# Optimization experiments

Hardware: AMD Instinct MI355X
Metric: run time of the kernel (lower is better)

## Reference

```python
import jax, jax.numpy as jnp
import numpy as np

EMBED_DIM = 1024
NUM_HEADS = 16
HEAD_DIM = EMBED_DIM // NUM_HEADS


def setup_inputs() -> dict:
    key = jax.random.key(0)
    k1, k2, k3 = jax.random.split(key, 3)
    B, S = 2, 2048
    scale_in = 1.0 / np.sqrt(EMBED_DIM)
    x = jax.random.normal(k1, (B, S, EMBED_DIM), dtype=jnp.float32)
    Wqkv = jax.random.normal(k2, (EMBED_DIM, 3 * EMBED_DIM), dtype=jnp.float32) * scale_in
    bqkv = jnp.zeros((3 * EMBED_DIM,), dtype=jnp.float32)
    Wout = jax.random.normal(k3, (EMBED_DIM, EMBED_DIM), dtype=jnp.float32) * scale_in
    bout = jnp.zeros((EMBED_DIM,), dtype=jnp.float32)
    return {"x": x, "Wqkv": Wqkv, "bqkv": bqkv, "Wout": Wout, "bout": bout}


def reference(x, Wqkv, bqkv, Wout, bout):
    # Causal multi-head self-attention (dropout in eval mode = identity).
    B, S, E = x.shape
    qkv = x @ Wqkv + bqkv                                  # [B,S,3E]
    qkv = qkv.reshape(B, S, 3, NUM_HEADS, HEAD_DIM)
    qkv = jnp.transpose(qkv, (2, 0, 3, 1, 4))              # [3,B,H,S,D]
    q, k, v = qkv[0], qkv[1], qkv[2]
    scores = jnp.einsum("bhqd,bhkd->bhqk", q, k) / np.sqrt(HEAD_DIM)
    causal = jnp.tril(jnp.ones((S, S), dtype=bool))
    scores = jnp.where(causal, scores, -jnp.inf)
    attn = jax.nn.softmax(scores, axis=-1)                 # [B,H,S,S]
    out = jnp.einsum("bhqk,bhkd->bhqd", attn, v)           # [B,H,S,D]
    out = jnp.transpose(out, (0, 2, 1, 3)).reshape(B, S, E)
    return out @ Wout + bout
```

## Files before the change

kernel.cpp:

```cpp
#include <hip/hip_runtime.h>
#include <hip/hip_bf16.h>

#define BB 2
#define SS 2048
#define EE 1024
#define HH 16
#define DD 64
#define MT (BB*SS)
#define NQ (3*EE)

typedef unsigned short u16;
typedef __bf16 bf16t;
typedef bf16t bf16x8 __attribute__((ext_vector_type(8)));
typedef short short8v __attribute__((ext_vector_type(8)));
typedef float f32x4 __attribute__((ext_vector_type(4)));

#define AS1 __attribute__((address_space(1)))
#define AS3 __attribute__((address_space(3)))

__device__ __forceinline__ u16 f2b(float f) {
  unsigned u = __builtin_bit_cast(unsigned, f);
  u += 0x7FFF + ((u >> 16) & 1);
  return (u16)(u >> 16);
}

__device__ __forceinline__ unsigned cvtpk(float lo, float hi) {
  unsigned r;
  asm("v_cvt_pk_bf16_f32 %0, %1, %2" : "=v"(r) : "v"(lo), "v"(hi));
  return r;
}

__device__ __forceinline__ void gload_lds16(const void* g, void* l) {
  __builtin_amdgcn_global_load_lds((const AS1 void*)(g), (AS3 void*)(l), 16, 0, 0);
}

__device__ __forceinline__ f32x4 mfma_bf16(short8v a, short8v b, f32x4 c) {
  return __builtin_amdgcn_mfma_f32_16x16x32_bf16(
      __builtin_bit_cast(bf16x8, a), __builtin_bit_cast(bf16x8, b), c, 0, 0, 0);
}

#define QSCALE 0.18033688f

__global__ void __launch_bounds__(256) cast_kernel(const float* __restrict__ in,
                                                   u16* __restrict__ out, int n) {
  int i = (blockIdx.x * 256 + threadIdx.x) * 4;
  if (i + 3 < n) {
    float4 v = *(const float4*)(in + i);
    ushort4 o;
    o.x = f2b(v.x); o.y = f2b(v.y); o.z = f2b(v.z); o.w = f2b(v.w);
    *(ushort4*)(out + i) = o;
  }
}

__global__ void __launch_bounds__(256) transpose_kernel(const float* __restrict__ W,
                                                        u16* __restrict__ WT,
                                                        int K, int N) {
  __shared__ float t[64][65];
  int k0 = blockIdx.y * 64, n0 = blockIdx.x * 64;
  int r = threadIdx.x >> 4;
  int c4 = (threadIdx.x & 15) * 4;
#pragma unroll
  for (int i = 0; i < 4; ++i) {
    float4 v = *(const float4*)(W + (size_t)(k0 + r + i * 16) * N + n0 + c4);
    t[r + i * 16][c4 + 0] = v.x; t[r + i * 16][c4 + 1] = v.y;
    t[r + i * 16][c4 + 2] = v.z; t[r + i * 16][c4 + 3] = v.w;
  }
  __syncthreads();
#pragma unroll
  for (int i = 0; i < 4; ++i) {
    ushort4 o;
    o.x = f2b(t[c4 + 0][r + i * 16]); o.y = f2b(t[c4 + 1][r + i * 16]);
    o.z = f2b(t[c4 + 2][r + i * 16]); o.w = f2b(t[c4 + 3][r + i * 16]);
    *(ushort4*)(WT + (size_t)(n0 + r + i * 16) * K + k0 + c4) = o;
  }
}

__global__ void __launch_bounds__(256) gemm_qkv_kernel(
    const u16* __restrict__ A, const u16* __restrict__ BT,
    const float* __restrict__ bias,
    u16* __restrict__ Qs, u16* __restrict__ Ks, u16* __restrict__ Vt) {
  __shared__ u16 As[8192];
  __shared__ u16 Bs[8192];
  const int K = EE;
  int tid = threadIdx.x;
  int w = tid >> 6, lane = tid & 63;
  int g = lane >> 4, q = lane & 15;
  int m0 = blockIdx.y * 128, n0 = blockIdx.x * 128;
  int wm = (w >> 1) * 64, wn = (w & 1) * 64;

  f32x4 acc[4][4] = {};

  int r = tid >> 2;
  int kc = (tid & 3) * 8;
  const u16* ga = A + (size_t)(m0 + r) * K + kc;
  const u16* gb = BT + (size_t)(n0 + r) * K + kc;
  u16* lA0 = As + w * 512;
  u16* lA1 = As + 2048 + w * 512;
  u16* lB0 = Bs + w * 512;
  u16* lB1 = Bs + 2048 + w * 512;

  gload_lds16(ga, lA0);
  gload_lds16(ga + 64 * K, lA1);
  gload_lds16(gb, lB0);
  gload_lds16(gb + 64 * K, lB1);
  ga += 32; gb += 32;
  __syncthreads();

  int cur = 0;
  for (int k0 = 0; k0 < K; k0 += 32) {
    if (k0 + 32 < K) {
      int nx = (cur ^ 1) * 4096;
      gload_lds16(ga, lA0 + nx);
      gload_lds16(ga + 64 * K, lA1 + nx);
      gload_lds16(gb, lB0 + nx);
      gload_lds16(gb + 64 * K, lB1 + nx);
      ga += 32; gb += 32;
    }
    const u16* Ab = As + cur * 4096;
    const u16* Bb = Bs + cur * 4096;
    short8v af[4], bfv[4];
#pragma unroll
    for (int m = 0; m < 4; ++m)
      af[m] = *(const short8v*)(Ab + (wm + m * 16 + q) * 32 + g * 8);
#pragma unroll
    for (int n = 0; n < 4; ++n)
      bfv[n] = *(const short8v*)(Bb + (wn + n * 16 + q) * 32 + g * 8);
#pragma unroll
    for (int m = 0; m < 4; ++m)
#pragma unroll
      for (int n = 0; n < 4; ++n)
        acc[m][n] = mfma_bf16(af[m], bfv[n], acc[m][n]);
    __syncthreads();
    cur ^= 1;
  }

#pragma unroll
  for (int m = 0; m < 4; ++m) {
    int row0 = m0 + wm + m * 16 + g * 4;
#pragma unroll
    for (int n = 0; n < 4; ++n) {
      int col = n0 + wn + n * 16 + q;
      float bi = bias[col];
      int t = col >> 10;
      int h = (col >> 6) & 15;
      int d = col & 63;
      int b = row0 >> 11, s0 = row0 & 2047;
      size_t bh = (size_t)b * HH + h;
      if (t == 2) {
        ushort4 vv;
        vv.x = f2b(acc[m][n][0] + bi); vv.y = f2b(acc[m][n][1] + bi);
        vv.z = f2b(acc[m][n][2] + bi); vv.w = f2b(acc[m][n][3] + bi);
        *(ushort4*)&Vt[(bh * DD + d) * SS + s0] = vv;
      } else if (t == 0) {
#pragma unroll
        for (int r2 = 0; r2 < 4; ++r2)
          Qs[(bh * SS + s0 + r2) * DD + d] = f2b((acc[m][n][r2] + bi) * QSCALE);
      } else {
#pragma unroll
        for (int r2 = 0; r2 < 4; ++r2)
          Ks[(bh * SS + s0 + r2) * DD + d] = f2b(acc[m][n][r2] + bi);
      }
    }
  }
}

__global__ void __launch_bounds__(512) attn_kernel(
    const u16* __restrict__ Qg, const u16* __restrict__ Kg,
    const u16* __restrict__ Vg, u16* __restrict__ O) {
  __shared__ char lds[49152];
  const int tid = threadIdx.x;
  const int w = tid >> 6, lane = tid & 63;
  const int g = lane >> 4, q = lane & 15;
  const int bid = blockIdx.x;
  const int bh = bid & 31;
  const int p = 15 - (bid >> 5);
  const int b = bh >> 4, h = bh & 15;
  char* Pw = lds + 32768 + w * 2048;
  const int qsw = (q & 7) << 4;

  const char* Qp = (const char*)Qg + (size_t)bh * (SS * 128);
  const char* Kp = (const char*)Kg + (size_t)bh * (SS * 128);
  const char* Vp = (const char*)Vg + (size_t)bh * (SS * 128);

  const int srow = tid >> 3;
  const int ssw = ((tid & 7) * 16) ^ ((srow & 7) << 4);
  const char* Ksrc = Kp + srow * 128 + ssw;
  const char* Vsrc = Vp + (size_t)srow * (SS * 2) + ssw;
  char* Kdst = lds + w * 1024;
  char* Vdst = lds + 16384 + w * 1024;

  const int nt = 2 * p + 2;
  const int qw = p * 128 + w * 16;

  short8v aq0 = *(const short8v*)(Qp + (size_t)(qw + q) * 128 + g * 16);
  short8v aq1 = *(const short8v*)(Qp + (size_t)(qw + q) * 128 + 64 + g * 16);

  f32x4 oacc[4] = {};
  float mrun = -1e30f, lrun = 0.f;

  gload_lds16(Ksrc, Kdst);
  gload_lds16(Vsrc, Vdst);
  __syncthreads();

  for (int s = 0; s < nt; ++s) {
    const int buf = s & 1;
    if (s + 1 < nt) {
      gload_lds16(Ksrc + (size_t)(s + 1) * 8192, Kdst + (buf ^ 1) * 8192);
      gload_lds16(Vsrc + (s + 1) * 128, Vdst + (buf ^ 1) * 8192);
    }
    const int kv0 = s << 6;
    if (kv0 <= qw + 15) {
      const char* Kc = lds + buf * 8192;
      const char* Vc = lds + 16384 + buf * 8192;
      short8v kf[4][2];
#pragma unroll
      for (int cc = 0; cc < 4; ++cc) {
        const char* kb = Kc + (cc * 16 + q) * 128;
        kf[cc][0] = *(const short8v*)(kb + ((g * 16) ^ qsw));
        kf[cc][1] = *(const short8v*)(kb + ((64 + g * 16) ^ qsw));
      }
      f32x4 st[4];
#pragma unroll
      for (int cc = 0; cc < 4; ++cc) {
        f32x4 z = {};
        z = mfma_bf16(kf[cc][0], aq0, z);
        z = mfma_bf16(kf[cc][1], aq1, z);
        st[cc] = z;
      }
      short8v vf[4][2];
#pragma unroll
      for (int v = 0; v < 4; ++v) {
        const char* vb = Vc + (v * 16 + q) * 128;
        vf[v][0] = *(const short8v*)(vb + ((g * 16) ^ qsw));
        vf[v][1] = *(const short8v*)(vb + ((64 + g * 16) ^ qsw));
      }
      if (kv0 + 63 > qw) {
        int row = qw + q;
#pragma unroll
        for (int cc = 0; cc < 4; ++cc) {
          int kvb = kv0 + cc * 16 + g * 4;
#pragma unroll
          for (int r2 = 0; r2 < 4; ++r2)
            if (kvb + r2 > row) st[cc][r2] = -1e30f;
        }
      }
      f32x4 t01, t23;
#pragma unroll
      for (int r2 = 0; r2 < 4; ++r2) {
        t01[r2] = fmaxf(st[0][r2], st[1][r2]);
        t23[r2] = fmaxf(st[2][r2], st[3][r2]);
      }
      float mx = fmaxf(fmaxf(fmaxf(t01[0], t01[1]), fmaxf(t01[2], t01[3])),
                       fmaxf(fmaxf(t23[0], t23[1]), fmaxf(t23[2], t23[3])));
      mx = fmaxf(mx, __shfl_xor(mx, 16));
      mx = fmaxf(mx, __shfl_xor(mx, 32));
      if (!__all(mx - mrun <= 8.f)) {
        float mnew = fmaxf(mrun, mx);
        float alpha = exp2f(mrun - mnew);
        mrun = mnew;
        lrun *= alpha;
#pragma unroll
        for (int vfi = 0; vfi < 4; ++vfi)
#pragma unroll
          for (int r2 = 0; r2 < 4; ++r2) oacc[vfi][r2] *= alpha;
      }
      f32x4 sum4 = {};
#pragma unroll
      for (int cc = 0; cc < 4; ++cc)
#pragma unroll
        for (int r2 = 0; r2 < 4; ++r2) {
          float pv = exp2f(st[cc][r2] - mrun);
          st[cc][r2] = pv;
          sum4[r2] += pv;
        }
      float sm = (sum4[0] + sum4[1]) + (sum4[2] + sum4[3]);
      sm += __shfl_xor(sm, 16);
      sm += __shfl_xor(sm, 32);
      lrun += sm;
      char* basep = Pw + q * 128;
#pragma unroll
      for (int cc = 0; cc < 4; ++cc) {
        unsigned p01 = cvtpk(st[cc][0], st[cc][1]);
        unsigned p23 = cvtpk(st[cc][2], st[cc][3]);
        *(unsigned*)(basep + ((32 * cc + 8 * g + 0) ^ qsw)) = p01;
        *(unsigned*)(basep + ((32 * cc + 8 * g + 4) ^ qsw)) = p23;
      }
      short8v pa0 = *(const short8v*)(basep + ((g * 16) ^ qsw));
      short8v pa1 = *(const short8v*)(basep + ((64 + g * 16) ^ qsw));
#pragma unroll
      for (int vfi = 0; vfi < 4; ++vfi) {
        oacc[vfi] = mfma_bf16(vf[vfi][0], pa0, oacc[vfi]);
        oacc[vfi] = mfma_bf16(vf[vfi][1], pa1, oacc[vfi]);
      }
    }
    __syncthreads();
  }

  {
    float inv = 1.0f / lrun;
    int row = qw + q;
    char* obase = (char*)O + (((size_t)b * SS + row) * EE + h * 64) * 2;
#pragma unroll
    for (int vfi = 0; vfi < 4; ++vfi) {
      uint2 o;
      o.x = cvtpk(oacc[vfi][0] * inv, oacc[vfi][1] * inv);
      o.y = cvtpk(oacc[vfi][2] * inv, oacc[vfi][3] * inv);
      *(uint2*)(obase + (vfi * 16 + g * 4) * 2) = o;
    }
  }
}

__global__ void __launch_bounds__(256) gemm_out_kernel(
    const u16* __restrict__ A, const u16* __restrict__ BT,
    const float* __restrict__ bias, float* __restrict__ Cout) {
  __shared__ u16 As[8192];
  __shared__ u16 Bs[8192];
  const int K = EE;
  int tid = threadIdx.x;
  int w = tid >> 6, lane = tid & 63;
  int g = lane >> 4, q = lane & 15;
  int m0 = blockIdx.y * 128, n0 = blockIdx.x * 128;
  int wm = (w >> 1) * 64, wn = (w & 1) * 64;

  f32x4 acc[4][4] = {};

  int r = tid >> 2;
  int kc = (tid & 3) * 8;
  const u16* ga = A + (size_t)(m0 + r) * K + kc;
  const u16* gb = BT + (size_t)(n0 + r) * K + kc;
  u16* lA0 = As + w * 512;
  u16* lA1 = As + 2048 + w * 512;
  u16* lB0 = Bs + w * 512;
  u16* lB1 = Bs + 2048 + w * 512;

  gload_lds16(ga, lA0);
  gload_lds16(ga + 64 * K, lA1);
  gload_lds16(gb, lB0);
  gload_lds16(gb + 64 * K, lB1);
  ga += 32; gb += 32;
  __syncthreads();

  int cur = 0;
  for (int k0 = 0; k0 < K; k0 += 32) {
    if (k0 + 32 < K) {
      int nx = (cur ^ 1) * 4096;
      gload_lds16(ga, lA0 + nx);
      gload_lds16(ga + 64 * K, lA1 + nx);
      gload_lds16(gb, lB0 + nx);
      gload_lds16(gb + 64 * K, lB1 + nx);
      ga += 32; gb += 32;
    }
    const u16* Ab = As + cur * 4096;
    const u16* Bb = Bs + cur * 4096;
    short8v af[4], bfv[4];
#pragma unroll
    for (int m = 0; m < 4; ++m)
      af[m] = *(const short8v*)(Ab + (wm + m * 16 + q) * 32 + g * 8);
#pragma unroll
    for (int n = 0; n < 4; ++n)
      bfv[n] = *(const short8v*)(Bb + (wn + n * 16 + q) * 32 + g * 8);
#pragma unroll
    for (int m = 0; m < 4; ++m)
#pragma unroll
      for (int n = 0; n < 4; ++n)
        acc[m][n] = mfma_bf16(af[m], bfv[n], acc[m][n]);
    __syncthreads();
    cur ^= 1;
  }

#pragma unroll
  for (int m = 0; m < 4; ++m) {
    int row0 = m0 + wm + m * 16 + g * 4;
#pragma unroll
    for (int n = 0; n < 4; ++n) {
      int col = n0 + wn + n * 16 + q;
      float bi = bias[col];
#pragma unroll
      for (int r2 = 0; r2 < 4; ++r2) {
        int row = row0 + r2;
        Cout[(size_t)row * EE + col] = acc[m][n][r2] + bi;
      }
    }
  }
}

extern "C" void kernel_launch(void* const* d_in, const int* in_sizes, int n_in,
                              void* d_out, int out_size, void* d_ws, size_t ws_size,
                              hipStream_t stream) {
  (void)in_sizes; (void)n_in; (void)out_size; (void)ws_size;
  const float* x    = (const float*)d_in[0];
  const float* Wqkv = (const float*)d_in[1];
  const float* bqkv = (const float*)d_in[2];
  const float* Wout = (const float*)d_in[3];
  const float* bout = (const float*)d_in[4];
  float* out = (float*)d_out;

  char* p = (char*)d_ws;
  u16* xb  = (u16*)p; p += (size_t)MT * EE * 2;
  u16* wqT = (u16*)p; p += (size_t)NQ * EE * 2;
  u16* woT = (u16*)p; p += (size_t)EE * EE * 2;
  u16* Qs  = (u16*)p; p += (size_t)BB * HH * SS * DD * 2;
  u16* Ks  = (u16*)p; p += (size_t)BB * HH * SS * DD * 2;
  u16* Vt  = (u16*)p; p += (size_t)BB * HH * DD * SS * 2;
  u16* Ob  = (u16*)p; p += (size_t)MT * EE * 2;

  cast_kernel<<<dim3((MT * EE / 4) / 256), dim3(256), 0, stream>>>(x, xb, MT * EE);
  transpose_kernel<<<dim3(NQ / 64, EE / 64), dim3(256), 0, stream>>>(Wqkv, wqT, EE, NQ);
  transpose_kernel<<<dim3(EE / 64, EE / 64), dim3(256), 0, stream>>>(Wout, woT, EE, EE);
  gemm_qkv_kernel<<<dim3(NQ / 128, MT / 128), dim3(256), 0, stream>>>(xb, wqT, bqkv, Qs, Ks, Vt);
  attn_kernel<<<dim3(512), dim3(512), 0, stream>>>(Qs, Ks, Vt, Ob);
  gemm_out_kernel<<<dim3(EE / 128, MT / 128), dim3(256), 0, stream>>>(Ob, woT, bout, out);
}
```

Measured before the change: 121.1 us.

## Split KV range across two wave halves with paired causal chunks and LDS merge

The attention kernel now uses 1024-thread blocks (256 blocks). Each block processes two 256-row query chunks (c and 7-c) so every block does the same amount of causal work. Within a block the two halves of the waves each take half of the KV tiles, and their softmax states and partial outputs are merged through LDS at the end. Each wave now handles 32 query rows, so every K/V fragment read from LDS feeds twice the MFMA work. In exchange it needs about 98KB of LDS and more registers per thread, adds merge synchronisation, and launches fewer, larger blocks, which may lower occupancy.

```diff
diff --git a/kernel.cpp b/kernel.cpp
--- a/kernel.cpp
+++ b/kernel.cpp
@@ -164,149 +164,196 @@
   }
 }
 
-__global__ void __launch_bounds__(512) attn_kernel(
+__global__ void __launch_bounds__(1024) attn_kernel(
     const u16* __restrict__ Qg, const u16* __restrict__ Kg,
     const u16* __restrict__ Vg, u16* __restrict__ O) {
-  __shared__ char lds[49152];
+  __shared__ char lds[100352];
   const int tid = threadIdx.x;
   const int w = tid >> 6, lane = tid & 63;
+  const int hv = w >> 3, ws = w & 7;
   const int g = lane >> 4, q = lane & 15;
   const int bid = blockIdx.x;
   const int bh = bid & 31;
-  const int p = 15 - (bid >> 5);
+  const int c0 = bid >> 5;
   const int b = bh >> 4, h = bh & 15;
-  char* Pw = lds + 32768 + w * 2048;
+  char* Pw = lds + 65536 + w * 2048;
   const int qsw = (q & 7) << 4;
 
   const char* Qp = (const char*)Qg + (size_t)bh * (SS * 128);
   const char* Kp = (const char*)Kg + (size_t)bh * (SS * 128);
   const char* Vp = (const char*)Vg + (size_t)bh * (SS * 128);
 
-  const int srow = tid >> 3;
-  const int ssw = ((tid & 7) * 16) ^ ((srow & 7) << 4);
+  const int tl = tid & 511;
+  const int srow = tl >> 3;
+  const int ssw = ((tl & 7) * 16) ^ ((srow & 7) << 4);
   const char* Ksrc = Kp + srow * 128 + ssw;
   const char* Vsrc = Vp + (size_t)srow * (SS * 2) + ssw;
-  char* Kdst = lds + w * 1024;
-  char* Vdst = lds + 16384 + w * 1024;
-
-  const int nt = 2 * p + 2;
-  const int qw = p * 128 + w * 16;
-
-  short8v aq0 = *(const short8v*)(Qp + (size_t)(qw + q) * 128 + g * 16);
-  short8v aq1 = *(const short8v*)(Qp + (size_t)(qw + q) * 128 + 64 + g * 16);
-
-  f32x4 oacc[4] = {};
-  float mrun = -1e30f, lrun = 0.f;
-
-  gload_lds16(Ksrc, Kdst);
-  gload_lds16(Vsrc, Vdst);
-  __syncthreads();
-
-  for (int s = 0; s < nt; ++s) {
-    const int buf = s & 1;
-    if (s + 1 < nt) {
-      gload_lds16(Ksrc + (size_t)(s + 1) * 8192, Kdst + (buf ^ 1) * 8192);
-      gload_lds16(Vsrc + (s + 1) * 128, Vdst + (buf ^ 1) * 8192);
-    }
-    const int kv0 = s << 6;
-    if (kv0 <= qw + 15) {
-      const char* Kc = lds + buf * 8192;
-      const char* Vc = lds + 16384 + buf * 8192;
-      short8v kf[4][2];
-#pragma unroll
-      for (int cc = 0; cc < 4; ++cc) {
-        const char* kb = Kc + (cc * 16 + q) * 128;
-        kf[cc][0] = *(const short8v*)(kb + ((g * 16) ^ qsw));
-        kf[cc][1] = *(const short8v*)(kb + ((64 + g * 16) ^ qsw));
-      }
-      f32x4 st[4];
-#pragma unroll
-      for (int cc = 0; cc < 4; ++cc) {
-        f32x4 z = {};
-        z = mfma_bf16(kf[cc][0], aq0, z);
-        z = mfma_bf16(kf[cc][1], aq1, z);
-        st[cc] = z;
-      }
-      short8v vf[4][2];
-#pragma unroll
-      for (int v = 0; v < 4; ++v) {
-        const char* vb = Vc + (v * 16 + q) * 128;
-        vf[v][0] = *(const short8v*)(vb + ((g * 16) ^ qsw));
-        vf[v][1] = *(const short8v*)(vb + ((64 + g * 16) ^ qsw));
-      }
-      if (kv0 + 63 > qw) {
-        int row = qw + q;
+  char* Kdst = lds + hv * 16384 + ws * 1024;
+  char* Vdst = lds + 32768 + hv * 16384 + ws * 1024;
+
+#pragma unroll 1
+  for (int pass = 0; pass < 2; ++pass) {
+    const int c = pass ? (7 - c0) : c0;
+    const int hl = 2 * (c + 1);
+    const int t0 = hv * hl;
+    const int qw = c * 256 + ws * 32;
+
+    short8v aq[2][2];
+#pragma unroll
+    for (int m = 0; m < 2; ++m)
+#pragma unroll
+      for (int j = 0; j < 2; ++j)
+        aq[m][j] = *(const short8v*)(Qp + (size_t)(qw + m * 16 + q) * 128 + j * 64 + g * 16);
+
+    f32x4 oacc[2][4] = {};
+    float mrun[2], lrun[2];
+#pragma unroll
+    for (int m = 0; m < 2; ++m) { mrun[m] = -1e30f; lrun[m] = 0.f; }
+
+    gload_lds16(Ksrc + (size_t)t0 * 8192, Kdst);
+    gload_lds16(Vsrc + t0 * 128, Vdst);
+    __syncthreads();
+
+    for (int s = 0; s < hl; ++s) {
+      const int buf = s & 1;
+      if (s + 1 < hl) {
+        gload_lds16(Ksrc + (size_t)(t0 + s + 1) * 8192, Kdst + (buf ^ 1) * 8192);
+        gload_lds16(Vsrc + (t0 + s + 1) * 128, Vdst + (buf ^ 1) * 8192);
+      }
+      const int kv0 = (t0 + s) << 6;
+      if (kv0 <= qw + 31) {
+        const char* Kc = lds + hv * 16384 + buf * 8192;
+        const char* Vc = lds + 32768 + hv * 16384 + buf * 8192;
+        short8v kf[4][2];
 #pragma unroll
         for (int cc = 0; cc < 4; ++cc) {
-          int kvb = kv0 + cc * 16 + g * 4;
-#pragma unroll
-          for (int r2 = 0; r2 < 4; ++r2)
-            if (kvb + r2 > row) st[cc][r2] = -1e30f;
+          const char* kb = Kc + (cc * 16 + q) * 128;
+          kf[cc][0] = *(const short8v*)(kb + ((g * 16) ^ qsw));
+          kf[cc][1] = *(const short8v*)(kb + ((64 + g * 16) ^ qsw));
         }
-      }
-      f32x4 t01, t23;
-#pragma unroll
-      for (int r2 = 0; r2 < 4; ++r2) {
-        t01[r2] = fmaxf(st[0][r2], st[1][r2]);
-        t23[r2] = fmaxf(st[2][r2], st[3][r2]);
-      }
-      float mx = fmaxf(fmaxf(fmaxf(t01[0], t01[1]), fmaxf(t01[2], t01[3])),
-                       fmaxf(fmaxf(t23[0], t23[1]), fmaxf(t23[2], t23[3])));
-      mx = fmaxf(mx, __shfl_xor(mx, 16));
-      mx = fmaxf(mx, __shfl_xor(mx, 32));
-      if (!__all(mx - mrun <= 8.f)) {
-        float mnew = fmaxf(mrun, mx);
-        float alpha = exp2f(mrun - mnew);
-        mrun = mnew;
-        lrun *= alpha;
+        f32x4 st[2][4];
+#pragma unroll
+        for (int m = 0; m < 2; ++m)
+#pragma unroll
+          for (int cc = 0; cc < 4; ++cc) {
+            f32x4 z = {};
+            z = mfma_bf16(kf[cc][0], aq[m][0], z);
+            z = mfma_bf16(kf[cc][1], aq[m][1], z);
+            st[m][cc] = z;
+          }
+        short8v vf[4][2];
+#pragma unroll
+        for (int v = 0; v < 4; ++v) {
+          const char* vb = Vc + (v * 16 + q) * 128;
+          vf[v][0] = *(const short8v*)(vb + ((g * 16) ^ qsw));
+          vf[v][1] = *(const short8v*)(vb + ((64 + g * 16) ^ qsw));
+        }
+        if (kv0 + 63 > qw) {
+#pragma unroll
+          for (int m = 0; m < 2; ++m) {
+            int row = qw + m * 16 + q;
+#pragma unroll
+            for (int cc = 0; cc < 4; ++cc) {
+              int kvb = kv0 + cc * 16 + g * 4;
+#pragma unroll
+              for (int r2 = 0; r2 < 4; ++r2)
+                if (kvb + r2 > row) st[m][cc][r2] = -1e30f;
+            }
+          }
+        }
+#pragma unroll
+        for (int m = 0; m < 2; ++m) {
+          f32x4 t01, t23;
+#pragma unroll
+          for (int r2 = 0; r2 < 4; ++r2) {
+            t01[r2] = fmaxf(st[m][0][r2], st[m][1][r2]);
+            t23[r2] = fmaxf(st[m][2][r2], st[m][3][r2]);
+          }
+          float mx = fmaxf(fmaxf(fmaxf(t01[0], t01[1]), fmaxf(t01[2], t01[3])),
+                           fmaxf(fmaxf(t23[0], t23[1]), fmaxf(t23[2], t23[3])));
+          mx = fmaxf(mx, __shfl_xor(mx, 16));
+          mx = fmaxf(mx, __shfl_xor(mx, 32));
+          if (!__all(mx - mrun[m] <= 8.f)) {
+            float mnew = fmaxf(mrun[m], mx);
+            float alpha = exp2f(mrun[m] - mnew);
+            mrun[m] = mnew;
+            lrun[m] *= alpha;
+#pragma unroll
+            for (int vfi = 0; vfi < 4; ++vfi)
+#pragma unroll
+              for (int r2 = 0; r2 < 4; ++r2) oacc[m][vfi][r2] *= alpha;
+          }
+          f32x4 sum4 = {};
+#pragma unroll
+          for (int cc = 0; cc < 4; ++cc)
+#pragma unroll
+            for (int r2 = 0; r2 < 4; ++r2) {
+              float pv = exp2f(st[m][cc][r2] - mrun[m]);
+              st[m][cc][r2] = pv;
+              sum4[r2] += pv;
+            }
+          float sm = (sum4[0] + sum4[1]) + (sum4[2] + sum4[3]);
+          sm += __shfl_xor(sm, 16);
+          sm += __shfl_xor(sm, 32);
+          lrun[m] += sm;
+          char* basep = Pw + q * 128;
+#pragma unroll
+          for (int cc = 0; cc < 4; ++cc) {
+            unsigned p01 = cvtpk(st[m][cc][0], st[m][cc][1]);
+            unsigned p23 = cvtpk(st[m][cc][2], st[m][cc][3]);
+            *(unsigned*)(basep + ((32 * cc + 8 * g + 0) ^ qsw)) = p01;
+            *(unsigned*)(basep + ((32 * cc + 8 * g + 4) ^ qsw)) = p23;
+          }
+          short8v pa0 = *(const short8v*)(basep + ((g * 16) ^ qsw));
+          short8v pa1 = *(const short8v*)(basep + ((64 + g * 16) ^ qsw));
+#pragma unroll
+          for (int vfi = 0; vfi < 4; ++vfi) {
+            oacc[m][vfi] = mfma_bf16(vf[vfi][0], pa0, oacc[m][vfi]);
+            oacc[m][vfi] = mfma_bf16(vf[vfi][1], pa1, oacc[m][vfi]);
+          }
+        }
+      }
+      __syncthreads();
+    }
+
+    if (hv) {
+      char* ob = lds + ws * 8192;
+#pragma unroll
+      for (int m = 0; m < 2; ++m) {
 #pragma unroll
         for (int vfi = 0; vfi < 4; ++vfi)
-#pragma unroll
-          for (int r2 = 0; r2 < 4; ++r2) oacc[vfi][r2] *= alpha;
-      }
-      f32x4 sum4 = {};
-#pragma unroll
-      for (int cc = 0; cc < 4; ++cc)
-#pragma unroll
-        for (int r2 = 0; r2 < 4; ++r2) {
-          float pv = exp2f(st[cc][r2] - mrun);
-          st[cc][r2] = pv;
-          sum4[r2] += pv;
+          *(f32x4*)(ob + (m * 4 + vfi) * 1024 + lane * 16) = oacc[m][vfi];
+        if (g == 0)
+          *(float2*)(lds + 98304 + (ws * 32 + m * 16 + q) * 8) =
+              make_float2(mrun[m], lrun[m]);
+      }
+    }
+    __syncthreads();
+    if (!hv) {
+      const char* ob = lds + ws * 8192;
+#pragma unroll
+      for (int m = 0; m < 2; ++m) {
+        float2 ml = *(const float2*)(lds + 98304 + (ws * 32 + m * 16 + q) * 8);
+        float mf = fmaxf(mrun[m], ml.x);
+        float a0 = exp2f(mrun[m] - mf);
+        float a1 = exp2f(ml.x - mf);
+        float inv = 1.0f / (a0 * lrun[m] + a1 * ml.y);
+        a0 *= inv; a1 *= inv;
+        int row = qw + m * 16 + q;
+        char* obase = (char*)O + (((size_t)b * SS + row) * EE + h * 64) * 2;
+#pragma unroll
+        for (int vfi = 0; vfi < 4; ++vfi) {
+          f32x4 o1 = *(const f32x4*)(ob + (m * 4 + vfi) * 1024 + lane * 16);
+          uint2 o;
+          o.x = cvtpk(a0 * oacc[m][vfi][0] + a1 * o1[0],
+                      a0 * oacc[m][vfi][1] + a1 * o1[1]);
+          o.y = cvtpk(a0 * oacc[m][vfi][2] + a1 * o1[2],
+                      a0 * oacc[m][vfi][3] + a1 * o1[3]);
+          *(uint2*)(obase + (vfi * 16 + g * 4) * 2) = o;
         }
-      float sm = (sum4[0] + sum4[1]) + (sum4[2] + sum4[3]);
-      sm += __shfl_xor(sm, 16);
-      sm += __shfl_xor(sm, 32);
-      lrun += sm;
-      char* basep = Pw + q * 128;
-#pragma unroll
-      for (int cc = 0; cc < 4; ++cc) {
-        unsigned p01 = cvtpk(st[cc][0], st[cc][1]);
-        unsigned p23 = cvtpk(st[cc][2], st[cc][3]);
-        *(unsigned*)(basep + ((32 * cc + 8 * g + 0) ^ qsw)) = p01;
-        *(unsigned*)(basep + ((32 * cc + 8 * g + 4) ^ qsw)) = p23;
-      }
-      short8v pa0 = *(const short8v*)(basep + ((g * 16) ^ qsw));
-      short8v pa1 = *(const short8v*)(basep + ((64 + g * 16) ^ qsw));
-#pragma unroll
-      for (int vfi = 0; vfi < 4; ++vfi) {
-        oacc[vfi] = mfma_bf16(vf[vfi][0], pa0, oacc[vfi]);
-        oacc[vfi] = mfma_bf16(vf[vfi][1], pa1, oacc[vfi]);
       }
     }
     __syncthreads();
-  }
-
-  {
-    float inv = 1.0f / lrun;
-    int row = qw + q;
-    char* obase = (char*)O + (((size_t)b * SS + row) * EE + h * 64) * 2;
-#pragma unroll
-    for (int vfi = 0; vfi < 4; ++vfi) {
-      uint2 o;
-      o.x = cvtpk(oacc[vfi][0] * inv, oacc[vfi][1] * inv);
-      o.y = cvtpk(oacc[vfi][2] * inv, oacc[vfi][3] * inv);
-      *(uint2*)(obase + (vfi * 16 + g * 4) * 2) = o;
-    }
   }
 }
 
@@ -408,6 +455,6 @@
   transpose_kernel<<<dim3(NQ / 64, EE / 64), dim3(256), 0, stream>>>(Wqkv, wqT, EE, NQ);
   transpose_kernel<<<dim3(EE / 64, EE / 64), dim3(256), 0, stream>>>(Wout, woT, EE, EE);
   gemm_qkv_kernel<<<dim3(NQ / 128, MT / 128), dim3(256), 0, stream>>>(xb, wqT, bqkv, Qs, Ks, Vt);
-  attn_kernel<<<dim3(512), dim3(512), 0, stream>>>(Qs, Ks, Vt, Ob);
+  attn_kernel<<<dim3(256), dim3(1024), 0, stream>>>(Qs, Ks, Vt, Ob);
   gemm_out_kernel<<<dim3(EE / 128, MT / 128), dim3(256), 0, stream>>>(Ob, woT, bout, out);
 }
```

New measurement: 247.1 us. 104% more time.
